# Kernel optimization log

Hardware: AMD Instinct MI355X
Metric: run time of the kernel (lower is better)

## Reference

```python
import jax, jax.numpy as jnp
import numpy as np

N = 32768       # batch of received vectors
N_RX = 8        # real-valued rx dimension (rows of G)
N_TX = 4        # n_tx_re
N_SYM = 4       # n_sym_re
K = N_SYM ** N_TX  # 256 joint symbol combos
SYMS = np.array([-3.0, -1.0, 1.0, 3.0]) / np.sqrt(5.0)  # 16-QAM real levels


def setup_inputs() -> dict:
    key = jax.random.key(0)
    k1, k2, k3, k4 = jax.random.split(key, 4)
    log_qi = jax.random.normal(k1, (N, N_TX, N_SYM), dtype=jnp.float32)
    G = jax.random.normal(k2, (N, N_RX, N_TX), dtype=jnp.float32)
    sqrt_2rho = jax.random.uniform(k3, (N,), dtype=jnp.float32, minval=0.5, maxval=2.0)
    n_var = jax.random.uniform(k4, (N,), dtype=jnp.float32, minval=0.05, maxval=0.5)
    # alpha is a NonNeg scalar weight (constant-initialized to 1.0). We use 0.8
    # (a plausible post-training value) so the (1-alpha)*log_qi path is exercised.
    alpha = jnp.float32(0.8)
    return {"log_qi": log_qi, "G": G, "sqrt_2rho": sqrt_2rho, "n_var": n_var, "alpha": alpha}


def _laplace_log_cdf(x):
    # Laplace(0,1): cdf = 0.5*exp(x) for x<0, 1 - 0.5*exp(-x) for x>=0
    return jnp.where(x < 0, x - jnp.log(2.0), jnp.log1p(-0.5 * jnp.exp(-jnp.abs(x))))


def reference(log_qi, G, sqrt_2rho, n_var, alpha):
    dt = log_qi.dtype
    syms = jnp.asarray(SYMS, dtype=dt)
    # All K = N_SYM**N_TX joint index combos (meshgrid 'ij' order = self.s_map order)
    grids = jnp.meshgrid(*([jnp.arange(N_SYM)] * N_TX), indexing='ij')
    idx = jnp.stack([g.reshape(-1) for g in grids], axis=-1)   # (K, N_TX) int
    s_all = syms[idx]                                          # (K, N_TX)

    # log p(y | s) for every joint combo: shared by all N_TX updates
    sG = sqrt_2rho[:, None, None] * G                          # (N, N_RX, N_TX)
    term = jnp.einsum('brt,kt->brk', sG, s_all)                # (N, N_RX, K)
    log_p = jnp.sum(_laplace_log_cdf(term), axis=1)            # (N, K)

    tx_ids = jnp.arange(N_TX)
    for xi in range(N_TX):  # unrolled Python loop, as in the original
        qi_un = jnp.exp(log_qi)
        qi = qi_un / jnp.sum(qi_un, axis=-1, keepdims=True)    # compute_qi
        # qi gathered at each combo: qi_sel[b,k,j] = qi[b, j, idx[k,j]]
        qi_sel = qi[:, tx_ids, idx]                            # (N, K, N_TX)
        # product over j != xi (row xi replaced by 1.0, as in tf.where insert)
        w = jnp.prod(jnp.where(tx_ids == xi, jnp.asarray(1.0, dt), qi_sel), axis=-1)  # (N, K)
        # group-sum combos by their xi-th symbol index
        onehot = (idx[:, xi][:, None] == jnp.arange(N_SYM)).astype(dt)  # (K, N_SYM)
        ex_log_qi = (w * log_p) @ onehot                       # (N, N_SYM)
        new_row = (1.0 - alpha) * log_qi[:, xi, :] + alpha * jax.lax.stop_gradient(ex_log_qi)
        log_qi = log_qi.at[:, xi, :].set(new_row)
        log_qi = log_qi - jax.lax.stop_gradient(jnp.max(log_qi, axis=-1, keepdims=True))
    return log_qi
```

## Files before the change

### kernel.cpp

```cpp
#include <hip/hip_runtime.h>

#define LOG2E 1.4426950408889634f
#define LN2F  0.6931471805599453f
#define RS5F  0.4472135954999579f

template<int XOR, int OR, int AND>
__device__ __forceinline__ float swz(float v) {
    return __int_as_float(__builtin_amdgcn_ds_swizzle(
        __float_as_int(v), (XOR << 10) | (OR << 5) | AND));
}
#define SWZX(v, m)     swz<(m), 0, 0x1F>(v)
#define BCAST16(v, s)  swz<0, (s), 0x10>(v)

__device__ __forceinline__ float sel4(float e0, float e1, float e2, float e3, int c) {
    float lo = (c & 1) ? e1 : e0;
    float hi = (c & 1) ? e3 : e2;
    return (c & 2) ? hi : lo;
}

__global__ __launch_bounds__(256) void mfnet_layer_kernel(
    const float* __restrict__ log_qi,
    const float* __restrict__ G,
    const float* __restrict__ sqrt_2rho,
    const float* __restrict__ alpha_ptr,
    float* __restrict__ out,
    int N)
{
    const int tid  = threadIdx.x;
    const int wv   = tid >> 6;
    const int lane = tid & 63;
    const int grp  = lane >> 4;
    const int u    = lane & 15;

    const int ib    = blockIdx.x * 16 + wv * 4;
    const int item0 = ib + grp;
    const bool valid = item0 < N;
    const int item  = valid ? item0 : (N - 1);

    __shared__ __align__(16) float sG[4][148];
    {
        size_t gidx = (size_t)ib * 32 + (size_t)(lane * 2);
        size_t gmax = (size_t)N * 32 - 2;
        if (gidx > gmax) gidx = gmax;
        const float2 gv = *(const float2*)(G + gidx);
        const int off = (lane * 2) & 31;
        *(float2*)&sG[wv][grp * 36 + off] = gv;
    }
    __syncthreads();

    const float rho   = sqrt_2rho[item];
    const float alpha = alpha_ptr[0];
    const float alm1  = 1.0f - alpha;
    const float rv    = rho * RS5F;

    const int c1 = u >> 2, c2 = u & 3;
    const float s1 = rv * (float)(2 * c1 - 3);
    const float s2 = rv * (float)(2 * c2 - 3);

    float slq2[16];
    {
        const float4* lq = (const float4*)(log_qi + (size_t)item * 16);
#pragma unroll
        for (int i = 0; i < 4; ++i) {
            float4 v = lq[i];
            slq2[4*i+0] = v.x * LOG2E; slq2[4*i+1] = v.y * LOG2E;
            slq2[4*i+2] = v.z * LOG2E; slq2[4*i+3] = v.w * LOG2E;
        }
    }

    float q1A, q1C, q2A, q2C, q3v0, q3v1, q3v2, q3v3;
    {
        float e0 = exp2f(slq2[4]), e1 = exp2f(slq2[5]), e2 = exp2f(slq2[6]), e3 = exp2f(slq2[7]);
        float inv = __builtin_amdgcn_rcpf(e0 + e1 + e2 + e3);
        q1A = sel4(e0, e1, e2, e3, c1) * inv;
        q1C = sel4(e0, e1, e2, e3, c1 ^ 3) * inv;
    }
    {
        float e0 = exp2f(slq2[8]), e1 = exp2f(slq2[9]), e2 = exp2f(slq2[10]), e3 = exp2f(slq2[11]);
        float inv = __builtin_amdgcn_rcpf(e0 + e1 + e2 + e3);
        q2A = sel4(e0, e1, e2, e3, c2) * inv;
        q2C = sel4(e0, e1, e2, e3, c2 ^ 3) * inv;
    }
    {
        float e0 = exp2f(slq2[12]), e1 = exp2f(slq2[13]), e2 = exp2f(slq2[14]), e3 = exp2f(slq2[15]);
        float inv = __builtin_amdgcn_rcpf(e0 + e1 + e2 + e3);
        q3v0 = e0 * inv; q3v1 = e1 * inv; q3v2 = e2 * inv; q3v3 = e3 * inv;
    }

    float lpA[8] = {0,0,0,0,0,0,0,0};
    float lpC[8] = {0,0,0,0,0,0,0,0};
    const float* gw = &sG[wv][grp * 36];
#pragma unroll
    for (int r = 0; r < 8; ++r) {
        float4 g = *(const float4*)(gw + r * 4);
        float b12 = fmaf(g.y, s1, g.z * s2);
        float m0  = g.x * rv;
        float m3  = g.w * rv;
        float t0  = fmaf(m0, -3.0f, b12);
        float t1  = b12 - m0;
#pragma unroll
        for (int j = 0; j < 8; ++j) {
            float tb = (j & 4) ? t1 : t0;
            float w3 = (float)(2 * (j & 3) - 3);
            float x  = fmaf(m3, w3, tb);
            float tt = fabsf(x) * (-LOG2E);
            float e  = exp2f(tt);
            float lg = __log2f(fmaf(e, -0.5f, 1.0f));
            float ng = tt - 1.0f;
            bool neg = (x < 0.0f);
            lpA[j] += neg ? ng : lg;
            lpC[j] += neg ? lg : ng;
        }
    }

    float ex0, ex1, ex2, ex3, m;
    float UA0 = lpA[0]*q3v0 + lpA[1]*q3v1 + lpA[2]*q3v2 + lpA[3]*q3v3;
    float UA1 = lpA[4]*q3v0 + lpA[5]*q3v1 + lpA[6]*q3v2 + lpA[7]*q3v3;
    float UC3 = lpC[0]*q3v3 + lpC[1]*q3v2 + lpC[2]*q3v1 + lpC[3]*q3v0;
    float UC2 = lpC[4]*q3v3 + lpC[5]*q3v2 + lpC[6]*q3v1 + lpC[7]*q3v0;

    {
        float preQ  = q1A * q2A;
        float preQC = q1C * q2C;
        float SA0 = UA0 * preQ, SA1 = UA1 * preQ;
        float SC2 = UC2 * preQC, SC3 = UC3 * preQC;
        SA0 += SWZX(SA0,1); SA0 += SWZX(SA0,2); SA0 += SWZX(SA0,4); SA0 += SWZX(SA0,8);
        SA1 += SWZX(SA1,1); SA1 += SWZX(SA1,2); SA1 += SWZX(SA1,4); SA1 += SWZX(SA1,8);
        SC2 += SWZX(SC2,1); SC2 += SWZX(SC2,2); SC2 += SWZX(SC2,4); SC2 += SWZX(SC2,8);
        SC3 += SWZX(SC3,1); SC3 += SWZX(SC3,2); SC3 += SWZX(SC3,4); SC3 += SWZX(SC3,8);
        ex0 = SA0; ex1 = SA1; ex2 = SC2; ex3 = SC3;
    }
    slq2[0] = alm1*slq2[0] + alpha*ex0;
    slq2[1] = alm1*slq2[1] + alpha*ex1;
    slq2[2] = alm1*slq2[2] + alpha*ex2;
    slq2[3] = alm1*slq2[3] + alpha*ex3;
#pragma unroll
    for (int t = 0; t < 4; ++t) {
        m = fmaxf(fmaxf(slq2[4*t], slq2[4*t+1]), fmaxf(slq2[4*t+2], slq2[4*t+3]));
        slq2[4*t] -= m; slq2[4*t+1] -= m; slq2[4*t+2] -= m; slq2[4*t+3] -= m;
    }
    float q0v0, q0v1, q0v2, q0v3;
    {
        float e0 = exp2f(slq2[0]), e1 = exp2f(slq2[1]), e2 = exp2f(slq2[2]), e3 = exp2f(slq2[3]);
        float inv = __builtin_amdgcn_rcpf(e0 + e1 + e2 + e3);
        q0v0 = e0*inv; q0v1 = e1*inv; q0v2 = e2*inv; q0v3 = e3*inv;
    }
    float IA = q0v0 * UA0 + q0v1 * UA1;
    float IC = q0v3 * UC3 + q0v2 * UC2;
    float Pin0 = lpA[0]*q0v0 + lpA[4]*q0v1;
    float Pin1 = lpA[1]*q0v0 + lpA[5]*q0v1;
    float Pin2 = lpA[2]*q0v0 + lpA[6]*q0v1;
    float Pin3 = lpA[3]*q0v0 + lpA[7]*q0v1;
    float Qin0 = lpC[3]*q0v3 + lpC[7]*q0v2;
    float Qin1 = lpC[2]*q0v3 + lpC[6]*q0v2;
    float Qin2 = lpC[1]*q0v3 + lpC[5]*q0v2;
    float Qin3 = lpC[0]*q0v3 + lpC[4]*q0v2;

    {
        float SA = q2A * IA;
        float SC = q2C * IC;
        SA += SWZX(SA,1); SA += SWZX(SA,2);
        SC += SWZX(SC,1); SC += SWZX(SC,2);
        float T = SA + SWZX(SC, 12);
        ex0 = BCAST16(T, 0); ex1 = BCAST16(T, 4); ex2 = BCAST16(T, 8); ex3 = BCAST16(T, 12);
        slq2[4] = alm1*slq2[4] + alpha*ex0;
        slq2[5] = alm1*slq2[5] + alpha*ex1;
        slq2[6] = alm1*slq2[6] + alpha*ex2;
        slq2[7] = alm1*slq2[7] + alpha*ex3;
        m = fmaxf(fmaxf(slq2[4], slq2[5]), fmaxf(slq2[6], slq2[7]));
        slq2[4] -= m; slq2[5] -= m; slq2[6] -= m; slq2[7] -= m;
        float e0 = exp2f(slq2[4]), e1 = exp2f(slq2[5]), e2 = exp2f(slq2[6]), e3 = exp2f(slq2[7]);
        float inv = __builtin_amdgcn_rcpf(e0 + e1 + e2 + e3);
        q1A = sel4(e0, e1, e2, e3, c1) * inv;
        q1C = sel4(e0, e1, e2, e3, c1 ^ 3) * inv;
    }

    {
        float SA = q1A * IA;
        float SC = q1C * IC;
        SA += SWZX(SA,4); SA += SWZX(SA,8);
        SC += SWZX(SC,4); SC += SWZX(SC,8);
        float T = SA + SWZX(SC, 3);
        ex0 = BCAST16(T, 0); ex1 = BCAST16(T, 1); ex2 = BCAST16(T, 2); ex3 = BCAST16(T, 3);
        slq2[8]  = alm1*slq2[8]  + alpha*ex0;
        slq2[9]  = alm1*slq2[9]  + alpha*ex1;
        slq2[10] = alm1*slq2[10] + alpha*ex2;
        slq2[11] = alm1*slq2[11] + alpha*ex3;
        m = fmaxf(fmaxf(slq2[8], slq2[9]), fmaxf(slq2[10], slq2[11]));
        slq2[8] -= m; slq2[9] -= m; slq2[10] -= m; slq2[11] -= m;
        float e0 = exp2f(slq2[8]), e1 = exp2f(slq2[9]), e2 = exp2f(slq2[10]), e3 = exp2f(slq2[11]);
        float inv = __builtin_amdgcn_rcpf(e0 + e1 + e2 + e3);
        q2A = sel4(e0, e1, e2, e3, c2) * inv;
        q2C = sel4(e0, e1, e2, e3, c2 ^ 3) * inv;
    }

    {
        float preQ  = q1A * q2A;
        float preQC = q1C * q2C;
        float R0 = Pin0 * preQ + Qin0 * preQC;
        float R1 = Pin1 * preQ + Qin1 * preQC;
        float R2 = Pin2 * preQ + Qin2 * preQC;
        float R3 = Pin3 * preQ + Qin3 * preQC;
        R0 += SWZX(R0,1); R0 += SWZX(R0,2); R0 += SWZX(R0,4); R0 += SWZX(R0,8);
        R1 += SWZX(R1,1); R1 += SWZX(R1,2); R1 += SWZX(R1,4); R1 += SWZX(R1,8);
        R2 += SWZX(R2,1); R2 += SWZX(R2,2); R2 += SWZX(R2,4); R2 += SWZX(R2,8);
        R3 += SWZX(R3,1); R3 += SWZX(R3,2); R3 += SWZX(R3,4); R3 += SWZX(R3,8);
        slq2[12] = alm1*slq2[12] + alpha*R0;
        slq2[13] = alm1*slq2[13] + alpha*R1;
        slq2[14] = alm1*slq2[14] + alpha*R2;
        slq2[15] = alm1*slq2[15] + alpha*R3;
        m = fmaxf(fmaxf(slq2[12], slq2[13]), fmaxf(slq2[14], slq2[15]));
        slq2[12] -= m; slq2[13] -= m; slq2[14] -= m; slq2[15] -= m;
    }

    if (valid) {
        float r0 = sel4(slq2[0],  slq2[1],  slq2[2],  slq2[3],  c2);
        float r1 = sel4(slq2[4],  slq2[5],  slq2[6],  slq2[7],  c2);
        float r2 = sel4(slq2[8],  slq2[9],  slq2[10], slq2[11], c2);
        float r3 = sel4(slq2[12], slq2[13], slq2[14], slq2[15], c2);
        float vv = sel4(r0, r1, r2, r3, c1);
        out[(size_t)item * 16 + u] = vv * LN2F;
    }
}

extern "C" void kernel_launch(void* const* d_in, const int* in_sizes, int n_in,
                              void* d_out, int out_size, void* d_ws, size_t ws_size,
                              hipStream_t stream) {
    const float* log_qi = (const float*)d_in[0];
    const float* G      = (const float*)d_in[1];
    const float* rho    = (const float*)d_in[2];
    const float* alpha  = (const float*)d_in[4];
    float* out = (float*)d_out;

    const int N = in_sizes[2];
    const int blocks = (N + 15) / 16;
    mfnet_layer_kernel<<<blocks, 256, 0, stream>>>(log_qi, G, rho, alpha, out, N);
}
```

Measured before the change: 85.42 us.

## Process two batch items per lane group to raise instruction-level parallelism

Each 16-lane group now handles two items instead of one, so a block covers 32 items and the grid is halved. G tiles are loaded as float4 into a larger shared buffer, and the __syncthreads after the shared-memory write is removed, since each wave reads only its own slice. The exp2, log2 and rcp calls now use raw amdgcn builtins, and launch bounds request 4 blocks per SM. The aim is to interleave two independent transcendental chains and cut per-item setup overhead, at the cost of more registers and lower occupancy.

```diff
diff --git a/kernel.cpp b/kernel.cpp
--- a/kernel.cpp
+++ b/kernel.cpp
@@ -11,6 +11,9 @@
 }
 #define SWZX(v, m)     swz<(m), 0, 0x1F>(v)
 #define BCAST16(v, s)  swz<0, (s), 0x10>(v)
+#define EXP2(x)  __builtin_amdgcn_exp2f(x)
+#define LOG2_(x) __builtin_amdgcn_logf(x)
+#define RCP_(x)  __builtin_amdgcn_rcpf(x)
 
 __device__ __forceinline__ float sel4(float e0, float e1, float e2, float e3, int c) {
     float lo = (c & 1) ? e1 : e0;
@@ -18,7 +21,7 @@
     return (c & 2) ? hi : lo;
 }
 
-__global__ __launch_bounds__(256) void mfnet_layer_kernel(
+__global__ __launch_bounds__(256, 4) void mfnet_layer_kernel(
     const float* __restrict__ log_qi,
     const float* __restrict__ G,
     const float* __restrict__ sqrt_2rho,
@@ -31,195 +34,218 @@
     const int lane = tid & 63;
     const int grp  = lane >> 4;
     const int u    = lane & 15;
-
-    const int ib    = blockIdx.x * 16 + wv * 4;
-    const int item0 = ib + grp;
-    const bool valid = item0 < N;
-    const int item  = valid ? item0 : (N - 1);
-
-    __shared__ __align__(16) float sG[4][148];
+    const int ib   = blockIdx.x * 32 + wv * 8;
+
+    __shared__ __align__(16) float sG[4][292];
     {
-        size_t gidx = (size_t)ib * 32 + (size_t)(lane * 2);
-        size_t gmax = (size_t)N * 32 - 2;
+        size_t gidx = (size_t)ib * 32 + (size_t)(lane * 4);
+        size_t gmax = (size_t)N * 32 - 4;
         if (gidx > gmax) gidx = gmax;
-        const float2 gv = *(const float2*)(G + gidx);
-        const int off = (lane * 2) & 31;
-        *(float2*)&sG[wv][grp * 36 + off] = gv;
-    }
-    __syncthreads();
-
-    const float rho   = sqrt_2rho[item];
+        const float4 gv = *(const float4*)(G + gidx);
+        *(float4*)&sG[wv][(lane >> 3) * 36 + ((lane * 4) & 31)] = gv;
+    }
+
     const float alpha = alpha_ptr[0];
     const float alm1  = 1.0f - alpha;
-    const float rv    = rho * RS5F;
-
     const int c1 = u >> 2, c2 = u & 3;
-    const float s1 = rv * (float)(2 * c1 - 3);
-    const float s2 = rv * (float)(2 * c2 - 3);
-
-    float slq2[16];
-    {
-        const float4* lq = (const float4*)(log_qi + (size_t)item * 16);
+
+    int   item[2]; bool valid[2];
+    float rv[2], s1v[2], s2v[2];
+    float slq2[2][16];
+#pragma unroll
+    for (int s = 0; s < 2; ++s) {
+        int it = ib + s * 4 + grp;
+        valid[s] = (it < N);
+        item[s]  = valid[s] ? it : (N - 1);
+        float rho = sqrt_2rho[item[s]];
+        rv[s]  = rho * RS5F;
+        s1v[s] = rv[s] * (float)(2 * c1 - 3);
+        s2v[s] = rv[s] * (float)(2 * c2 - 3);
+        const float4* lq = (const float4*)(log_qi + (size_t)item[s] * 16);
 #pragma unroll
         for (int i = 0; i < 4; ++i) {
             float4 v = lq[i];
-            slq2[4*i+0] = v.x * LOG2E; slq2[4*i+1] = v.y * LOG2E;
-            slq2[4*i+2] = v.z * LOG2E; slq2[4*i+3] = v.w * LOG2E;
-        }
-    }
-
-    float q1A, q1C, q2A, q2C, q3v0, q3v1, q3v2, q3v3;
-    {
-        float e0 = exp2f(slq2[4]), e1 = exp2f(slq2[5]), e2 = exp2f(slq2[6]), e3 = exp2f(slq2[7]);
-        float inv = __builtin_amdgcn_rcpf(e0 + e1 + e2 + e3);
-        q1A = sel4(e0, e1, e2, e3, c1) * inv;
-        q1C = sel4(e0, e1, e2, e3, c1 ^ 3) * inv;
-    }
-    {
-        float e0 = exp2f(slq2[8]), e1 = exp2f(slq2[9]), e2 = exp2f(slq2[10]), e3 = exp2f(slq2[11]);
-        float inv = __builtin_amdgcn_rcpf(e0 + e1 + e2 + e3);
-        q2A = sel4(e0, e1, e2, e3, c2) * inv;
-        q2C = sel4(e0, e1, e2, e3, c2 ^ 3) * inv;
-    }
-    {
-        float e0 = exp2f(slq2[12]), e1 = exp2f(slq2[13]), e2 = exp2f(slq2[14]), e3 = exp2f(slq2[15]);
-        float inv = __builtin_amdgcn_rcpf(e0 + e1 + e2 + e3);
-        q3v0 = e0 * inv; q3v1 = e1 * inv; q3v2 = e2 * inv; q3v3 = e3 * inv;
-    }
-
-    float lpA[8] = {0,0,0,0,0,0,0,0};
-    float lpC[8] = {0,0,0,0,0,0,0,0};
-    const float* gw = &sG[wv][grp * 36];
+            slq2[s][4*i+0] = v.x * LOG2E; slq2[s][4*i+1] = v.y * LOG2E;
+            slq2[s][4*i+2] = v.z * LOG2E; slq2[s][4*i+3] = v.w * LOG2E;
+        }
+    }
+
+    float q1A[2], q1C[2], q2A[2], q2C[2], q3v[2][4];
+#pragma unroll
+    for (int s = 0; s < 2; ++s) {
+        {
+            float e0 = EXP2(slq2[s][4]),  e1 = EXP2(slq2[s][5]);
+            float e2 = EXP2(slq2[s][6]),  e3 = EXP2(slq2[s][7]);
+            float inv = RCP_(e0 + e1 + e2 + e3);
+            q1A[s] = sel4(e0, e1, e2, e3, c1) * inv;
+            q1C[s] = sel4(e0, e1, e2, e3, c1 ^ 3) * inv;
+        }
+        {
+            float e0 = EXP2(slq2[s][8]),  e1 = EXP2(slq2[s][9]);
+            float e2 = EXP2(slq2[s][10]), e3 = EXP2(slq2[s][11]);
+            float inv = RCP_(e0 + e1 + e2 + e3);
+            q2A[s] = sel4(e0, e1, e2, e3, c2) * inv;
+            q2C[s] = sel4(e0, e1, e2, e3, c2 ^ 3) * inv;
+        }
+        {
+            float e0 = EXP2(slq2[s][12]), e1 = EXP2(slq2[s][13]);
+            float e2 = EXP2(slq2[s][14]), e3 = EXP2(slq2[s][15]);
+            float inv = RCP_(e0 + e1 + e2 + e3);
+            q3v[s][0] = e0*inv; q3v[s][1] = e1*inv;
+            q3v[s][2] = e2*inv; q3v[s][3] = e3*inv;
+        }
+    }
+
+    float lpA[2][8] = {{0,0,0,0,0,0,0,0},{0,0,0,0,0,0,0,0}};
+    float lpC[2][8] = {{0,0,0,0,0,0,0,0},{0,0,0,0,0,0,0,0}};
+    const float* gw[2] = { &sG[wv][grp * 36], &sG[wv][(4 + grp) * 36] };
 #pragma unroll
     for (int r = 0; r < 8; ++r) {
-        float4 g = *(const float4*)(gw + r * 4);
-        float b12 = fmaf(g.y, s1, g.z * s2);
-        float m0  = g.x * rv;
-        float m3  = g.w * rv;
-        float t0  = fmaf(m0, -3.0f, b12);
-        float t1  = b12 - m0;
-#pragma unroll
-        for (int j = 0; j < 8; ++j) {
-            float tb = (j & 4) ? t1 : t0;
-            float w3 = (float)(2 * (j & 3) - 3);
-            float x  = fmaf(m3, w3, tb);
-            float tt = fabsf(x) * (-LOG2E);
-            float e  = exp2f(tt);
-            float lg = __log2f(fmaf(e, -0.5f, 1.0f));
-            float ng = tt - 1.0f;
-            bool neg = (x < 0.0f);
-            lpA[j] += neg ? ng : lg;
-            lpC[j] += neg ? lg : ng;
-        }
-    }
-
-    float ex0, ex1, ex2, ex3, m;
-    float UA0 = lpA[0]*q3v0 + lpA[1]*q3v1 + lpA[2]*q3v2 + lpA[3]*q3v3;
-    float UA1 = lpA[4]*q3v0 + lpA[5]*q3v1 + lpA[6]*q3v2 + lpA[7]*q3v3;
-    float UC3 = lpC[0]*q3v3 + lpC[1]*q3v2 + lpC[2]*q3v1 + lpC[3]*q3v0;
-    float UC2 = lpC[4]*q3v3 + lpC[5]*q3v2 + lpC[6]*q3v1 + lpC[7]*q3v0;
-
-    {
-        float preQ  = q1A * q2A;
-        float preQC = q1C * q2C;
-        float SA0 = UA0 * preQ, SA1 = UA1 * preQ;
-        float SC2 = UC2 * preQC, SC3 = UC3 * preQC;
+#pragma unroll
+        for (int s = 0; s < 2; ++s) {
+            float4 g = *(const float4*)(gw[s] + r * 4);
+            float b12 = fmaf(g.y, s1v[s], g.z * s2v[s]);
+            float m0  = g.x * rv[s];
+            float m3  = g.w * rv[s];
+            float t0  = fmaf(m0, -3.0f, b12);
+            float t1  = b12 - m0;
+#pragma unroll
+            for (int j = 0; j < 8; ++j) {
+                float tb = (j & 4) ? t1 : t0;
+                float w3 = (float)(2 * (j & 3) - 3);
+                float x  = fmaf(m3, w3, tb);
+                float tt = fabsf(x) * (-LOG2E);
+                float e  = EXP2(tt);
+                float lg = LOG2_(fmaf(e, -0.5f, 1.0f));
+                float ng = tt - 1.0f;
+                bool neg = (x < 0.0f);
+                lpA[s][j] += neg ? ng : lg;
+                lpC[s][j] += neg ? lg : ng;
+            }
+        }
+    }
+
+    float UA0[2], UA1[2], UC2[2], UC3[2];
+#pragma unroll
+    for (int s = 0; s < 2; ++s) {
+        UA0[s] = lpA[s][0]*q3v[s][0] + lpA[s][1]*q3v[s][1] + lpA[s][2]*q3v[s][2] + lpA[s][3]*q3v[s][3];
+        UA1[s] = lpA[s][4]*q3v[s][0] + lpA[s][5]*q3v[s][1] + lpA[s][6]*q3v[s][2] + lpA[s][7]*q3v[s][3];
+        UC3[s] = lpC[s][0]*q3v[s][3] + lpC[s][1]*q3v[s][2] + lpC[s][2]*q3v[s][1] + lpC[s][3]*q3v[s][0];
+        UC2[s] = lpC[s][4]*q3v[s][3] + lpC[s][5]*q3v[s][2] + lpC[s][6]*q3v[s][1] + lpC[s][7]*q3v[s][0];
+    }
+
+    float IA[2], IC[2], Pin[2][4], Qin[2][4];
+#pragma unroll
+    for (int s = 0; s < 2; ++s) {
+        float preQ  = q1A[s] * q2A[s];
+        float preQC = q1C[s] * q2C[s];
+        float SA0 = UA0[s]*preQ,  SA1 = UA1[s]*preQ;
+        float SC2 = UC2[s]*preQC, SC3 = UC3[s]*preQC;
         SA0 += SWZX(SA0,1); SA0 += SWZX(SA0,2); SA0 += SWZX(SA0,4); SA0 += SWZX(SA0,8);
         SA1 += SWZX(SA1,1); SA1 += SWZX(SA1,2); SA1 += SWZX(SA1,4); SA1 += SWZX(SA1,8);
         SC2 += SWZX(SC2,1); SC2 += SWZX(SC2,2); SC2 += SWZX(SC2,4); SC2 += SWZX(SC2,8);
         SC3 += SWZX(SC3,1); SC3 += SWZX(SC3,2); SC3 += SWZX(SC3,4); SC3 += SWZX(SC3,8);
-        ex0 = SA0; ex1 = SA1; ex2 = SC2; ex3 = SC3;
-    }
-    slq2[0] = alm1*slq2[0] + alpha*ex0;
-    slq2[1] = alm1*slq2[1] + alpha*ex1;
-    slq2[2] = alm1*slq2[2] + alpha*ex2;
-    slq2[3] = alm1*slq2[3] + alpha*ex3;
-#pragma unroll
-    for (int t = 0; t < 4; ++t) {
-        m = fmaxf(fmaxf(slq2[4*t], slq2[4*t+1]), fmaxf(slq2[4*t+2], slq2[4*t+3]));
-        slq2[4*t] -= m; slq2[4*t+1] -= m; slq2[4*t+2] -= m; slq2[4*t+3] -= m;
-    }
-    float q0v0, q0v1, q0v2, q0v3;
-    {
-        float e0 = exp2f(slq2[0]), e1 = exp2f(slq2[1]), e2 = exp2f(slq2[2]), e3 = exp2f(slq2[3]);
-        float inv = __builtin_amdgcn_rcpf(e0 + e1 + e2 + e3);
-        q0v0 = e0*inv; q0v1 = e1*inv; q0v2 = e2*inv; q0v3 = e3*inv;
-    }
-    float IA = q0v0 * UA0 + q0v1 * UA1;
-    float IC = q0v3 * UC3 + q0v2 * UC2;
-    float Pin0 = lpA[0]*q0v0 + lpA[4]*q0v1;
-    float Pin1 = lpA[1]*q0v0 + lpA[5]*q0v1;
-    float Pin2 = lpA[2]*q0v0 + lpA[6]*q0v1;
-    float Pin3 = lpA[3]*q0v0 + lpA[7]*q0v1;
-    float Qin0 = lpC[3]*q0v3 + lpC[7]*q0v2;
-    float Qin1 = lpC[2]*q0v3 + lpC[6]*q0v2;
-    float Qin2 = lpC[1]*q0v3 + lpC[5]*q0v2;
-    float Qin3 = lpC[0]*q0v3 + lpC[4]*q0v2;
-
-    {
-        float SA = q2A * IA;
-        float SC = q2C * IC;
+        slq2[s][0] = alm1*slq2[s][0] + alpha*SA0;
+        slq2[s][1] = alm1*slq2[s][1] + alpha*SA1;
+        slq2[s][2] = alm1*slq2[s][2] + alpha*SC2;
+        slq2[s][3] = alm1*slq2[s][3] + alpha*SC3;
+#pragma unroll
+        for (int t = 0; t < 4; ++t) {
+            float m = fmaxf(fmaxf(slq2[s][4*t], slq2[s][4*t+1]),
+                            fmaxf(slq2[s][4*t+2], slq2[s][4*t+3]));
+            slq2[s][4*t] -= m; slq2[s][4*t+1] -= m;
+            slq2[s][4*t+2] -= m; slq2[s][4*t+3] -= m;
+        }
+        float e0 = EXP2(slq2[s][0]), e1 = EXP2(slq2[s][1]);
+        float e2 = EXP2(slq2[s][2]), e3 = EXP2(slq2[s][3]);
+        float inv = RCP_(e0 + e1 + e2 + e3);
+        float q0v0 = e0*inv, q0v1 = e1*inv, q0v2 = e2*inv, q0v3 = e3*inv;
+        IA[s] = q0v0 * UA0[s] + q0v1 * UA1[s];
+        IC[s] = q0v3 * UC3[s] + q0v2 * UC2[s];
+        Pin[s][0] = lpA[s][0]*q0v0 + lpA[s][4]*q0v1;
+        Pin[s][1] = lpA[s][1]*q0v0 + lpA[s][5]*q0v1;
+        Pin[s][2] = lpA[s][2]*q0v0 + lpA[s][6]*q0v1;
+        Pin[s][3] = lpA[s][3]*q0v0 + lpA[s][7]*q0v1;
+        Qin[s][0] = lpC[s][3]*q0v3 + lpC[s][7]*q0v2;
+        Qin[s][1] = lpC[s][2]*q0v3 + lpC[s][6]*q0v2;
+        Qin[s][2] = lpC[s][1]*q0v3 + lpC[s][5]*q0v2;
+        Qin[s][3] = lpC[s][0]*q0v3 + lpC[s][4]*q0v2;
+    }
+
+#pragma unroll
+    for (int s = 0; s < 2; ++s) {
+        float SA = q2A[s] * IA[s];
+        float SC = q2C[s] * IC[s];
         SA += SWZX(SA,1); SA += SWZX(SA,2);
         SC += SWZX(SC,1); SC += SWZX(SC,2);
         float T = SA + SWZX(SC, 12);
-        ex0 = BCAST16(T, 0); ex1 = BCAST16(T, 4); ex2 = BCAST16(T, 8); ex3 = BCAST16(T, 12);
-        slq2[4] = alm1*slq2[4] + alpha*ex0;
-        slq2[5] = alm1*slq2[5] + alpha*ex1;
-        slq2[6] = alm1*slq2[6] + alpha*ex2;
-        slq2[7] = alm1*slq2[7] + alpha*ex3;
-        m = fmaxf(fmaxf(slq2[4], slq2[5]), fmaxf(slq2[6], slq2[7]));
-        slq2[4] -= m; slq2[5] -= m; slq2[6] -= m; slq2[7] -= m;
-        float e0 = exp2f(slq2[4]), e1 = exp2f(slq2[5]), e2 = exp2f(slq2[6]), e3 = exp2f(slq2[7]);
-        float inv = __builtin_amdgcn_rcpf(e0 + e1 + e2 + e3);
-        q1A = sel4(e0, e1, e2, e3, c1) * inv;
-        q1C = sel4(e0, e1, e2, e3, c1 ^ 3) * inv;
-    }
-
-    {
-        float SA = q1A * IA;
-        float SC = q1C * IC;
+        float ex0 = BCAST16(T, 0),  ex1 = BCAST16(T, 4);
+        float ex2 = BCAST16(T, 8),  ex3 = BCAST16(T, 12);
+        slq2[s][4] = alm1*slq2[s][4] + alpha*ex0;
+        slq2[s][5] = alm1*slq2[s][5] + alpha*ex1;
+        slq2[s][6] = alm1*slq2[s][6] + alpha*ex2;
+        slq2[s][7] = alm1*slq2[s][7] + alpha*ex3;
+        float m = fmaxf(fmaxf(slq2[s][4], slq2[s][5]), fmaxf(slq2[s][6], slq2[s][7]));
+        slq2[s][4] -= m; slq2[s][5] -= m; slq2[s][6] -= m; slq2[s][7] -= m;
+        float e0 = EXP2(slq2[s][4]), e1 = EXP2(slq2[s][5]);
+        float e2 = EXP2(slq2[s][6]), e3 = EXP2(slq2[s][7]);
+        float inv = RCP_(e0 + e1 + e2 + e3);
+        q1A[s] = sel4(e0, e1, e2, e3, c1) * inv;
+        q1C[s] = sel4(e0, e1, e2, e3, c1 ^ 3) * inv;
+    }
+
+#pragma unroll
+    for (int s = 0; s < 2; ++s) {
+        float SA = q1A[s] * IA[s];
+        float SC = q1C[s] * IC[s];
         SA += SWZX(SA,4); SA += SWZX(SA,8);
         SC += SWZX(SC,4); SC += SWZX(SC,8);
         float T = SA + SWZX(SC, 3);
-        ex0 = BCAST16(T, 0); ex1 = BCAST16(T, 1); ex2 = BCAST16(T, 2); ex3 = BCAST16(T, 3);
-        slq2[8]  = alm1*slq2[8]  + alpha*ex0;
-        slq2[9]  = alm1*slq2[9]  + alpha*ex1;
-        slq2[10] = alm1*slq2[10] + alpha*ex2;
-        slq2[11] = alm1*slq2[11] + alpha*ex3;
-        m = fmaxf(fmaxf(slq2[8], slq2[9]), fmaxf(slq2[10], slq2[11]));
-        slq2[8] -= m; slq2[9] -= m; slq2[10] -= m; slq2[11] -= m;
-        float e0 = exp2f(slq2[8]), e1 = exp2f(slq2[9]), e2 = exp2f(slq2[10]), e3 = exp2f(slq2[11]);
-        float inv = __builtin_amdgcn_rcpf(e0 + e1 + e2 + e3);
-        q2A = sel4(e0, e1, e2, e3, c2) * inv;
-        q2C = sel4(e0, e1, e2, e3, c2 ^ 3) * inv;
-    }
-
-    {
-        float preQ  = q1A * q2A;
-        float preQC = q1C * q2C;
-        float R0 = Pin0 * preQ + Qin0 * preQC;
-        float R1 = Pin1 * preQ + Qin1 * preQC;
-        float R2 = Pin2 * preQ + Qin2 * preQC;
-        float R3 = Pin3 * preQ + Qin3 * preQC;
+        float ex0 = BCAST16(T, 0), ex1 = BCAST16(T, 1);
+        float ex2 = BCAST16(T, 2), ex3 = BCAST16(T, 3);
+        slq2[s][8]  = alm1*slq2[s][8]  + alpha*ex0;
+        slq2[s][9]  = alm1*slq2[s][9]  + alpha*ex1;
+        slq2[s][10] = alm1*slq2[s][10] + alpha*ex2;
+        slq2[s][11] = alm1*slq2[s][11] + alpha*ex3;
+        float m = fmaxf(fmaxf(slq2[s][8], slq2[s][9]), fmaxf(slq2[s][10], slq2[s][11]));
+        slq2[s][8] -= m; slq2[s][9] -= m; slq2[s][10] -= m; slq2[s][11] -= m;
+        float e0 = EXP2(slq2[s][8]),  e1 = EXP2(slq2[s][9]);
+        float e2 = EXP2(slq2[s][10]), e3 = EXP2(slq2[s][11]);
+        float inv = RCP_(e0 + e1 + e2 + e3);
+        q2A[s] = sel4(e0, e1, e2, e3, c2) * inv;
+        q2C[s] = sel4(e0, e1, e2, e3, c2 ^ 3) * inv;
+    }
+
+#pragma unroll
+    for (int s = 0; s < 2; ++s) {
+        float preQ  = q1A[s] * q2A[s];
+        float preQC = q1C[s] * q2C[s];
+        float R0 = Pin[s][0]*preQ + Qin[s][0]*preQC;
+        float R1 = Pin[s][1]*preQ + Qin[s][1]*preQC;
+        float R2 = Pin[s][2]*preQ + Qin[s][2]*preQC;
+        float R3 = Pin[s][3]*preQ + Qin[s][3]*preQC;
         R0 += SWZX(R0,1); R0 += SWZX(R0,2); R0 += SWZX(R0,4); R0 += SWZX(R0,8);
         R1 += SWZX(R1,1); R1 += SWZX(R1,2); R1 += SWZX(R1,4); R1 += SWZX(R1,8);
         R2 += SWZX(R2,1); R2 += SWZX(R2,2); R2 += SWZX(R2,4); R2 += SWZX(R2,8);
         R3 += SWZX(R3,1); R3 += SWZX(R3,2); R3 += SWZX(R3,4); R3 += SWZX(R3,8);
-        slq2[12] = alm1*slq2[12] + alpha*R0;
-        slq2[13] = alm1*slq2[13] + alpha*R1;
-        slq2[14] = alm1*slq2[14] + alpha*R2;
-        slq2[15] = alm1*slq2[15] + alpha*R3;
-        m = fmaxf(fmaxf(slq2[12], slq2[13]), fmaxf(slq2[14], slq2[15]));
-        slq2[12] -= m; slq2[13] -= m; slq2[14] -= m; slq2[15] -= m;
-    }
-
-    if (valid) {
-        float r0 = sel4(slq2[0],  slq2[1],  slq2[2],  slq2[3],  c2);
-        float r1 = sel4(slq2[4],  slq2[5],  slq2[6],  slq2[7],  c2);
-        float r2 = sel4(slq2[8],  slq2[9],  slq2[10], slq2[11], c2);
-        float r3 = sel4(slq2[12], slq2[13], slq2[14], slq2[15], c2);
-        float vv = sel4(r0, r1, r2, r3, c1);
-        out[(size_t)item * 16 + u] = vv * LN2F;
+        slq2[s][12] = alm1*slq2[s][12] + alpha*R0;
+        slq2[s][13] = alm1*slq2[s][13] + alpha*R1;
+        slq2[s][14] = alm1*slq2[s][14] + alpha*R2;
+        slq2[s][15] = alm1*slq2[s][15] + alpha*R3;
+        float m = fmaxf(fmaxf(slq2[s][12], slq2[s][13]), fmaxf(slq2[s][14], slq2[s][15]));
+        slq2[s][12] -= m; slq2[s][13] -= m; slq2[s][14] -= m; slq2[s][15] -= m;
+    }
+
+#pragma unroll
+    for (int s = 0; s < 2; ++s) {
+        if (valid[s]) {
+            float r0 = sel4(slq2[s][0],  slq2[s][1],  slq2[s][2],  slq2[s][3],  c2);
+            float r1 = sel4(slq2[s][4],  slq2[s][5],  slq2[s][6],  slq2[s][7],  c2);
+            float r2 = sel4(slq2[s][8],  slq2[s][9],  slq2[s][10], slq2[s][11], c2);
+            float r3 = sel4(slq2[s][12], slq2[s][13], slq2[s][14], slq2[s][15], c2);
+            float vv = sel4(r0, r1, r2, r3, c1);
+            out[(size_t)item[s] * 16 + u] = vv * LN2F;
+        }
     }
 }
 
@@ -233,6 +259,6 @@
     float* out = (float*)d_out;
 
     const int N = in_sizes[2];
-    const int blocks = (N + 15) / 16;
+    const int blocks = (N + 31) / 32;
     mfnet_layer_kernel<<<blocks, 256, 0, stream>>>(log_qi, G, rho, alpha, out, N);
 }
```

Result: slower. 87.35 us (+2.3%).

## Spread each item over 32 lanes so each lane evaluates four symbol combos

Applied to the files above, without the earlier changes.

Each batch item now uses 32 lanes instead of 16, with the extra lane bit selecting the first transmit symbol. Each lane evaluates 4 Laplace log-CDF combos per row instead of 8, and the launch uses twice as many blocks. The swizzle reductions and broadcasts are reworked for the 32-lane layout, and the block-wide barrier after the shared G load is dropped. The kernel also calls raw exp2/log/rcp builtins and adds an occupancy hint to launch_bounds. The aim is more parallelism and shorter per-lane dependency chains, at the cost of longer cross-lane reduction trees and half the lanes sitting idle on the final store.

```diff
diff --git a/kernel.cpp b/kernel.cpp
--- a/kernel.cpp
+++ b/kernel.cpp
@@ -9,8 +9,11 @@
     return __int_as_float(__builtin_amdgcn_ds_swizzle(
         __float_as_int(v), (XOR << 10) | (OR << 5) | AND));
 }
-#define SWZX(v, m)     swz<(m), 0, 0x1F>(v)
-#define BCAST16(v, s)  swz<0, (s), 0x10>(v)
+#define SWZX(v, m)    swz<(m), 0, 0x1F>(v)
+#define BCAST32(v, s) swz<0, (s), 0>(v)
+#define EXP2(x)  __builtin_amdgcn_exp2f(x)
+#define LOG2_(x) __builtin_amdgcn_logf(x)
+#define RCP_(x)  __builtin_amdgcn_rcpf(x)
 
 __device__ __forceinline__ float sel4(float e0, float e1, float e2, float e3, int c) {
     float lo = (c & 1) ? e1 : e0;
@@ -18,7 +21,7 @@
     return (c & 2) ? hi : lo;
 }
 
-__global__ __launch_bounds__(256) void mfnet_layer_kernel(
+__global__ __launch_bounds__(256, 8) void mfnet_layer_kernel(
     const float* __restrict__ log_qi,
     const float* __restrict__ G,
     const float* __restrict__ sqrt_2rho,
@@ -29,33 +32,34 @@
     const int tid  = threadIdx.x;
     const int wv   = tid >> 6;
     const int lane = tid & 63;
-    const int grp  = lane >> 4;
-    const int u    = lane & 15;
-
-    const int ib    = blockIdx.x * 16 + wv * 4;
-    const int item0 = ib + grp;
-    const bool valid = item0 < N;
-    const int item  = valid ? item0 : (N - 1);
-
-    __shared__ __align__(16) float sG[4][148];
-    {
-        size_t gidx = (size_t)ib * 32 + (size_t)(lane * 2);
-        size_t gmax = (size_t)N * 32 - 2;
+    const int grp  = lane >> 5;
+    const int u    = lane & 31;
+    const int ib   = blockIdx.x * 8 + wv * 2;
+
+    __shared__ __align__(16) float sG[4][64];
+    {
+        size_t gidx = (size_t)ib * 32 + (size_t)lane;
+        size_t gmax = (size_t)N * 32 - 1;
         if (gidx > gmax) gidx = gmax;
-        const float2 gv = *(const float2*)(G + gidx);
-        const int off = (lane * 2) & 31;
-        *(float2*)&sG[wv][grp * 36 + off] = gv;
-    }
-    __syncthreads();
-
-    const float rho   = sqrt_2rho[item];
+        sG[wv][lane] = G[gidx];
+    }
+
+    const int it0   = ib + grp;
+    const bool valid = (it0 < N);
+    const int item  = valid ? it0 : (N - 1);
+
     const float alpha = alpha_ptr[0];
     const float alm1  = 1.0f - alpha;
-    const float rv    = rho * RS5F;
-
-    const int c1 = u >> 2, c2 = u & 3;
-    const float s1 = rv * (float)(2 * c1 - 3);
-    const float s2 = rv * (float)(2 * c2 - 3);
+
+    const int bit0 = u & 1;
+    const int c2   = (u >> 1) & 3;
+    const int c1   = (u >> 3) & 3;
+
+    const float rho = sqrt_2rho[item];
+    const float rv  = rho * RS5F;
+    const float s1  = rv * (float)(2 * c1 - 3);
+    const float s2  = rv * (float)(2 * c2 - 3);
+    const float w0  = rv * (float)(2 * bit0 - 3);
 
     float slq2[16];
     {
@@ -70,42 +74,41 @@
 
     float q1A, q1C, q2A, q2C, q3v0, q3v1, q3v2, q3v3;
     {
-        float e0 = exp2f(slq2[4]), e1 = exp2f(slq2[5]), e2 = exp2f(slq2[6]), e3 = exp2f(slq2[7]);
-        float inv = __builtin_amdgcn_rcpf(e0 + e1 + e2 + e3);
+        float e0 = EXP2(slq2[4]),  e1 = EXP2(slq2[5]);
+        float e2 = EXP2(slq2[6]),  e3 = EXP2(slq2[7]);
+        float inv = RCP_(e0 + e1 + e2 + e3);
         q1A = sel4(e0, e1, e2, e3, c1) * inv;
         q1C = sel4(e0, e1, e2, e3, c1 ^ 3) * inv;
     }
     {
-        float e0 = exp2f(slq2[8]), e1 = exp2f(slq2[9]), e2 = exp2f(slq2[10]), e3 = exp2f(slq2[11]);
-        float inv = __builtin_amdgcn_rcpf(e0 + e1 + e2 + e3);
+        float e0 = EXP2(slq2[8]),  e1 = EXP2(slq2[9]);
+        float e2 = EXP2(slq2[10]), e3 = EXP2(slq2[11]);
+        float inv = RCP_(e0 + e1 + e2 + e3);
         q2A = sel4(e0, e1, e2, e3, c2) * inv;
         q2C = sel4(e0, e1, e2, e3, c2 ^ 3) * inv;
     }
     {
-        float e0 = exp2f(slq2[12]), e1 = exp2f(slq2[13]), e2 = exp2f(slq2[14]), e3 = exp2f(slq2[15]);
-        float inv = __builtin_amdgcn_rcpf(e0 + e1 + e2 + e3);
-        q3v0 = e0 * inv; q3v1 = e1 * inv; q3v2 = e2 * inv; q3v3 = e3 * inv;
-    }
-
-    float lpA[8] = {0,0,0,0,0,0,0,0};
-    float lpC[8] = {0,0,0,0,0,0,0,0};
-    const float* gw = &sG[wv][grp * 36];
+        float e0 = EXP2(slq2[12]), e1 = EXP2(slq2[13]);
+        float e2 = EXP2(slq2[14]), e3 = EXP2(slq2[15]);
+        float inv = RCP_(e0 + e1 + e2 + e3);
+        q3v0 = e0*inv; q3v1 = e1*inv; q3v2 = e2*inv; q3v3 = e3*inv;
+    }
+
+    float lpA[4] = {0,0,0,0};
+    float lpC[4] = {0,0,0,0};
+    const float* gw = &sG[wv][grp * 32];
 #pragma unroll
     for (int r = 0; r < 8; ++r) {
         float4 g = *(const float4*)(gw + r * 4);
-        float b12 = fmaf(g.y, s1, g.z * s2);
-        float m0  = g.x * rv;
-        float m3  = g.w * rv;
-        float t0  = fmaf(m0, -3.0f, b12);
-        float t1  = b12 - m0;
-#pragma unroll
-        for (int j = 0; j < 8; ++j) {
-            float tb = (j & 4) ? t1 : t0;
-            float w3 = (float)(2 * (j & 3) - 3);
+        float tb = fmaf(g.x, w0, fmaf(g.y, s1, g.z * s2));
+        float m3 = g.w * rv;
+#pragma unroll
+        for (int j = 0; j < 4; ++j) {
+            float w3 = (float)(2 * j - 3);
             float x  = fmaf(m3, w3, tb);
             float tt = fabsf(x) * (-LOG2E);
-            float e  = exp2f(tt);
-            float lg = __log2f(fmaf(e, -0.5f, 1.0f));
+            float e  = EXP2(tt);
+            float lg = LOG2_(fmaf(e, -0.5f, 1.0f));
             float ng = tt - 1.0f;
             bool neg = (x < 0.0f);
             lpA[j] += neg ? ng : lg;
@@ -113,64 +116,57 @@
         }
     }
 
-    float ex0, ex1, ex2, ex3, m;
-    float UA0 = lpA[0]*q3v0 + lpA[1]*q3v1 + lpA[2]*q3v2 + lpA[3]*q3v3;
-    float UA1 = lpA[4]*q3v0 + lpA[5]*q3v1 + lpA[6]*q3v2 + lpA[7]*q3v3;
-    float UC3 = lpC[0]*q3v3 + lpC[1]*q3v2 + lpC[2]*q3v1 + lpC[3]*q3v0;
-    float UC2 = lpC[4]*q3v3 + lpC[5]*q3v2 + lpC[6]*q3v1 + lpC[7]*q3v0;
-
-    {
-        float preQ  = q1A * q2A;
-        float preQC = q1C * q2C;
-        float SA0 = UA0 * preQ, SA1 = UA1 * preQ;
-        float SC2 = UC2 * preQC, SC3 = UC3 * preQC;
-        SA0 += SWZX(SA0,1); SA0 += SWZX(SA0,2); SA0 += SWZX(SA0,4); SA0 += SWZX(SA0,8);
-        SA1 += SWZX(SA1,1); SA1 += SWZX(SA1,2); SA1 += SWZX(SA1,4); SA1 += SWZX(SA1,8);
-        SC2 += SWZX(SC2,1); SC2 += SWZX(SC2,2); SC2 += SWZX(SC2,4); SC2 += SWZX(SC2,8);
-        SC3 += SWZX(SC3,1); SC3 += SWZX(SC3,2); SC3 += SWZX(SC3,4); SC3 += SWZX(SC3,8);
-        ex0 = SA0; ex1 = SA1; ex2 = SC2; ex3 = SC3;
-    }
-    slq2[0] = alm1*slq2[0] + alpha*ex0;
-    slq2[1] = alm1*slq2[1] + alpha*ex1;
-    slq2[2] = alm1*slq2[2] + alpha*ex2;
-    slq2[3] = alm1*slq2[3] + alpha*ex3;
-#pragma unroll
-    for (int t = 0; t < 4; ++t) {
-        m = fmaxf(fmaxf(slq2[4*t], slq2[4*t+1]), fmaxf(slq2[4*t+2], slq2[4*t+3]));
-        slq2[4*t] -= m; slq2[4*t+1] -= m; slq2[4*t+2] -= m; slq2[4*t+3] -= m;
-    }
-    float q0v0, q0v1, q0v2, q0v3;
-    {
-        float e0 = exp2f(slq2[0]), e1 = exp2f(slq2[1]), e2 = exp2f(slq2[2]), e3 = exp2f(slq2[3]);
-        float inv = __builtin_amdgcn_rcpf(e0 + e1 + e2 + e3);
-        q0v0 = e0*inv; q0v1 = e1*inv; q0v2 = e2*inv; q0v3 = e3*inv;
-    }
-    float IA = q0v0 * UA0 + q0v1 * UA1;
-    float IC = q0v3 * UC3 + q0v2 * UC2;
-    float Pin0 = lpA[0]*q0v0 + lpA[4]*q0v1;
-    float Pin1 = lpA[1]*q0v0 + lpA[5]*q0v1;
-    float Pin2 = lpA[2]*q0v0 + lpA[6]*q0v1;
-    float Pin3 = lpA[3]*q0v0 + lpA[7]*q0v1;
-    float Qin0 = lpC[3]*q0v3 + lpC[7]*q0v2;
-    float Qin1 = lpC[2]*q0v3 + lpC[6]*q0v2;
-    float Qin2 = lpC[1]*q0v3 + lpC[5]*q0v2;
-    float Qin3 = lpC[0]*q0v3 + lpC[4]*q0v2;
+    float UA = lpA[0]*q3v0 + lpA[1]*q3v1 + lpA[2]*q3v2 + lpA[3]*q3v3;
+    float UC = lpC[0]*q3v3 + lpC[1]*q3v2 + lpC[2]*q3v1 + lpC[3]*q3v0;
+
+    float q0A, q0C, IA, IC;
+    {
+        float SA = UA * (q1A * q2A);
+        float SC = UC * (q1C * q2C);
+        SA += SWZX(SA,2); SA += SWZX(SA,4); SA += SWZX(SA,8); SA += SWZX(SA,16);
+        SC += SWZX(SC,2); SC += SWZX(SC,4); SC += SWZX(SC,8); SC += SWZX(SC,16);
+        float SAo = SWZX(SA,1), SCo = SWZX(SC,1);
+        float ex0 = bit0 ? SAo : SA;
+        float ex1 = bit0 ? SA  : SAo;
+        float ex2 = bit0 ? SC  : SCo;
+        float ex3 = bit0 ? SCo : SC;
+        slq2[0] = alm1*slq2[0] + alpha*ex0;
+        slq2[1] = alm1*slq2[1] + alpha*ex1;
+        slq2[2] = alm1*slq2[2] + alpha*ex2;
+        slq2[3] = alm1*slq2[3] + alpha*ex3;
+#pragma unroll
+        for (int t = 0; t < 4; ++t) {
+            float m = fmaxf(fmaxf(slq2[4*t], slq2[4*t+1]),
+                            fmaxf(slq2[4*t+2], slq2[4*t+3]));
+            slq2[4*t] -= m; slq2[4*t+1] -= m;
+            slq2[4*t+2] -= m; slq2[4*t+3] -= m;
+        }
+        float e0 = EXP2(slq2[0]), e1 = EXP2(slq2[1]);
+        float e2 = EXP2(slq2[2]), e3 = EXP2(slq2[3]);
+        float inv = RCP_(e0 + e1 + e2 + e3);
+        q0A = (bit0 ? e1 : e0) * inv;
+        q0C = (bit0 ? e2 : e3) * inv;
+        IA = q0A * UA;
+        IC = q0C * UC;
+    }
 
     {
         float SA = q2A * IA;
         float SC = q2C * IC;
-        SA += SWZX(SA,1); SA += SWZX(SA,2);
-        SC += SWZX(SC,1); SC += SWZX(SC,2);
-        float T = SA + SWZX(SC, 12);
-        ex0 = BCAST16(T, 0); ex1 = BCAST16(T, 4); ex2 = BCAST16(T, 8); ex3 = BCAST16(T, 12);
+        SA += SWZX(SA,1); SA += SWZX(SA,2); SA += SWZX(SA,4);
+        SC += SWZX(SC,1); SC += SWZX(SC,2); SC += SWZX(SC,4);
+        float T = SA + SWZX(SC, 24);
+        float ex0 = BCAST32(T, 0),  ex1 = BCAST32(T, 8);
+        float ex2 = BCAST32(T, 16), ex3 = BCAST32(T, 24);
         slq2[4] = alm1*slq2[4] + alpha*ex0;
         slq2[5] = alm1*slq2[5] + alpha*ex1;
         slq2[6] = alm1*slq2[6] + alpha*ex2;
         slq2[7] = alm1*slq2[7] + alpha*ex3;
-        m = fmaxf(fmaxf(slq2[4], slq2[5]), fmaxf(slq2[6], slq2[7]));
+        float m = fmaxf(fmaxf(slq2[4], slq2[5]), fmaxf(slq2[6], slq2[7]));
         slq2[4] -= m; slq2[5] -= m; slq2[6] -= m; slq2[7] -= m;
-        float e0 = exp2f(slq2[4]), e1 = exp2f(slq2[5]), e2 = exp2f(slq2[6]), e3 = exp2f(slq2[7]);
-        float inv = __builtin_amdgcn_rcpf(e0 + e1 + e2 + e3);
+        float e0 = EXP2(slq2[4]), e1 = EXP2(slq2[5]);
+        float e2 = EXP2(slq2[6]), e3 = EXP2(slq2[7]);
+        float inv = RCP_(e0 + e1 + e2 + e3);
         q1A = sel4(e0, e1, e2, e3, c1) * inv;
         q1C = sel4(e0, e1, e2, e3, c1 ^ 3) * inv;
     }
@@ -178,47 +174,50 @@
     {
         float SA = q1A * IA;
         float SC = q1C * IC;
-        SA += SWZX(SA,4); SA += SWZX(SA,8);
-        SC += SWZX(SC,4); SC += SWZX(SC,8);
-        float T = SA + SWZX(SC, 3);
-        ex0 = BCAST16(T, 0); ex1 = BCAST16(T, 1); ex2 = BCAST16(T, 2); ex3 = BCAST16(T, 3);
+        SA += SWZX(SA,1); SA += SWZX(SA,8); SA += SWZX(SA,16);
+        SC += SWZX(SC,1); SC += SWZX(SC,8); SC += SWZX(SC,16);
+        float T = SA + SWZX(SC, 6);
+        float ex0 = BCAST32(T, 0), ex1 = BCAST32(T, 2);
+        float ex2 = BCAST32(T, 4), ex3 = BCAST32(T, 6);
         slq2[8]  = alm1*slq2[8]  + alpha*ex0;
         slq2[9]  = alm1*slq2[9]  + alpha*ex1;
         slq2[10] = alm1*slq2[10] + alpha*ex2;
         slq2[11] = alm1*slq2[11] + alpha*ex3;
-        m = fmaxf(fmaxf(slq2[8], slq2[9]), fmaxf(slq2[10], slq2[11]));
+        float m = fmaxf(fmaxf(slq2[8], slq2[9]), fmaxf(slq2[10], slq2[11]));
         slq2[8] -= m; slq2[9] -= m; slq2[10] -= m; slq2[11] -= m;
-        float e0 = exp2f(slq2[8]), e1 = exp2f(slq2[9]), e2 = exp2f(slq2[10]), e3 = exp2f(slq2[11]);
-        float inv = __builtin_amdgcn_rcpf(e0 + e1 + e2 + e3);
+        float e0 = EXP2(slq2[8]),  e1 = EXP2(slq2[9]);
+        float e2 = EXP2(slq2[10]), e3 = EXP2(slq2[11]);
+        float inv = RCP_(e0 + e1 + e2 + e3);
         q2A = sel4(e0, e1, e2, e3, c2) * inv;
         q2C = sel4(e0, e1, e2, e3, c2 ^ 3) * inv;
     }
 
     {
-        float preQ  = q1A * q2A;
-        float preQC = q1C * q2C;
-        float R0 = Pin0 * preQ + Qin0 * preQC;
-        float R1 = Pin1 * preQ + Qin1 * preQC;
-        float R2 = Pin2 * preQ + Qin2 * preQC;
-        float R3 = Pin3 * preQ + Qin3 * preQC;
-        R0 += SWZX(R0,1); R0 += SWZX(R0,2); R0 += SWZX(R0,4); R0 += SWZX(R0,8);
-        R1 += SWZX(R1,1); R1 += SWZX(R1,2); R1 += SWZX(R1,4); R1 += SWZX(R1,8);
-        R2 += SWZX(R2,1); R2 += SWZX(R2,2); R2 += SWZX(R2,4); R2 += SWZX(R2,8);
-        R3 += SWZX(R3,1); R3 += SWZX(R3,2); R3 += SWZX(R3,4); R3 += SWZX(R3,8);
+        float WA = q0A * q1A * q2A;
+        float WC = q0C * q1C * q2C;
+        float R0 = lpA[0]*WA + lpC[3]*WC;
+        float R1 = lpA[1]*WA + lpC[2]*WC;
+        float R2 = lpA[2]*WA + lpC[1]*WC;
+        float R3 = lpA[3]*WA + lpC[0]*WC;
+        R0 += SWZX(R0,1); R0 += SWZX(R0,2); R0 += SWZX(R0,4); R0 += SWZX(R0,8); R0 += SWZX(R0,16);
+        R1 += SWZX(R1,1); R1 += SWZX(R1,2); R1 += SWZX(R1,4); R1 += SWZX(R1,8); R1 += SWZX(R1,16);
+        R2 += SWZX(R2,1); R2 += SWZX(R2,2); R2 += SWZX(R2,4); R2 += SWZX(R2,8); R2 += SWZX(R2,16);
+        R3 += SWZX(R3,1); R3 += SWZX(R3,2); R3 += SWZX(R3,4); R3 += SWZX(R3,8); R3 += SWZX(R3,16);
         slq2[12] = alm1*slq2[12] + alpha*R0;
         slq2[13] = alm1*slq2[13] + alpha*R1;
         slq2[14] = alm1*slq2[14] + alpha*R2;
         slq2[15] = alm1*slq2[15] + alpha*R3;
-        m = fmaxf(fmaxf(slq2[12], slq2[13]), fmaxf(slq2[14], slq2[15]));
+        float m = fmaxf(fmaxf(slq2[12], slq2[13]), fmaxf(slq2[14], slq2[15]));
         slq2[12] -= m; slq2[13] -= m; slq2[14] -= m; slq2[15] -= m;
     }
 
-    if (valid) {
-        float r0 = sel4(slq2[0],  slq2[1],  slq2[2],  slq2[3],  c2);
-        float r1 = sel4(slq2[4],  slq2[5],  slq2[6],  slq2[7],  c2);
-        float r2 = sel4(slq2[8],  slq2[9],  slq2[10], slq2[11], c2);
-        float r3 = sel4(slq2[12], slq2[13], slq2[14], slq2[15], c2);
-        float vv = sel4(r0, r1, r2, r3, c1);
+    if (valid && u < 16) {
+        const int c = u & 3;
+        float r0 = sel4(slq2[0],  slq2[1],  slq2[2],  slq2[3],  c);
+        float r1 = sel4(slq2[4],  slq2[5],  slq2[6],  slq2[7],  c);
+        float r2 = sel4(slq2[8],  slq2[9],  slq2[10], slq2[11], c);
+        float r3 = sel4(slq2[12], slq2[13], slq2[14], slq2[15], c);
+        float vv = sel4(r0, r1, r2, r3, u >> 2);
         out[(size_t)item * 16 + u] = vv * LN2F;
     }
 }
@@ -233,6 +232,6 @@
     float* out = (float*)d_out;
 
     const int N = in_sizes[2];
-    const int blocks = (N + 15) / 16;
+    const int blocks = (N + 7) / 8;
     mfnet_layer_kernel<<<blocks, 256, 0, stream>>>(log_qi, G, rho, alpha, out, N);
 }
```

Result: no change. 84.63 us (-0.9%).
